# Kernel optimization log

Hardware: AMD Instinct MI355X
Metric: run time of the kernel (lower is better)

The kernel has to match this reference:

```python
import jax, jax.numpy as jnp
import numpy as np

B, T, D, H = 256, 512, 512, 512


def setup_inputs() -> dict:
    key = jax.random.key(0)
    k0, k1, k2, k3 = jax.random.split(key, 4)
    sD = 1.0 / np.sqrt(D).astype(np.float32)
    sH = 1.0 / np.sqrt(H).astype(np.float32)
    return {
        "x": jax.random.normal(k0, (B, T, D), jnp.float32),
        "Wx": jax.random.normal(k1, (D, 4 * H), jnp.float32) * sD,
        "Wh": jax.random.normal(k2, (H, 4 * H), jnp.float32) * sH,
        "b": jnp.zeros((4 * H,), jnp.float32),
        "Wfc": jax.random.normal(k3, (H, 1), jnp.float32) * sH,
        "bfc": jnp.zeros((1,), jnp.float32),
    }


def reference(x, Wx, Wh, b, Wfc, bfc):
    # x: [B, T, D]. Flax LSTMCell gates (i, f, g, o):
    #   i,f,o = sigmoid(.), g = tanh(.); c' = f*c + i*g; h' = o*tanh(c')
    Bv, Tv, _ = x.shape
    Hv = Wh.shape[0]
    # Precompute all input projections in one big GEMM (same math, batched).
    xg = jnp.einsum('btd,dg->btg', x, Wx) + b  # [B, T, 4H]

    def step(carry, xt):
        c, h = carry
        gates = xt + h @ Wh                     # [B, 4H]
        i, f, g, o = jnp.split(gates, 4, axis=-1)
        c_new = jax.nn.sigmoid(f) * c + jax.nn.sigmoid(i) * jnp.tanh(g)
        h_new = jax.nn.sigmoid(o) * jnp.tanh(c_new)
        return (c_new, h_new), None

    c0 = jnp.zeros((Bv, Hv), x.dtype)
    h0 = jnp.zeros((Bv, Hv), x.dtype)
    (c_fin, h_fin), _ = jax.lax.scan(step, (c0, h0), jnp.swapaxes(xg, 0, 1))
    # fc applied to last timestep output (== final hidden state)
    return h_fin @ Wfc + bfc  # [B, 1]
```

## Files before the change

### kernel.cpp

```cpp
#include <hip/hip_runtime.h>
#include <hip/hip_bf16.h>


typedef _Float16 half8 __attribute__((ext_vector_type(8)));
typedef _Float16 half4 __attribute__((ext_vector_type(4)));
typedef int int4v __attribute__((ext_vector_type(4)));
typedef float float4v __attribute__((ext_vector_type(4)));

__device__ __forceinline__ void gl_lds16(const void* g, void* l) {
  __builtin_amdgcn_global_load_lds(
      (const __attribute__((address_space(1))) unsigned int*)g,
      (__attribute__((address_space(3))) unsigned int*)l, 16, 0, 0);
}

__device__ __forceinline__ float sigm(float v) { return 1.f / (1.f + __expf(-v)); }
__device__ __forceinline__ float tanh_(float v) { return 1.f - 2.f / (__expf(2.f * v) + 1.f); }

__global__ __launch_bounds__(256) void k_prep(
    const float* __restrict__ x, const float* __restrict__ Wx,
    const float* __restrict__ Wh, const float* __restrict__ b,
    _Float16* __restrict__ xf, _Float16* __restrict__ wxt,
    _Float16* __restrict__ wht, float* __restrict__ bp)
{
  const long NX8 = 67108864L / 8;
  const long NW  = 2048L * 512;
  const long TOT = NX8 + 2 * NW + 2048;
  long stride = (long)gridDim.x * blockDim.x;
  for (long id = (long)blockIdx.x * blockDim.x + threadIdx.x; id < TOT; id += stride) {
    if (id < NX8) {
      const float4v* p = (const float4v*)x + id * 2;
      float4v a = p[0], c = p[1];
      half8 o;
      o[0]=(_Float16)a[0]; o[1]=(_Float16)a[1]; o[2]=(_Float16)a[2]; o[3]=(_Float16)a[3];
      o[4]=(_Float16)c[0]; o[5]=(_Float16)c[1]; o[6]=(_Float16)c[2]; o[7]=(_Float16)c[3];
      ((half8*)xf)[id] = o;
    } else if (id < NX8 + NW) {
      long e = id - NX8;
      int np = (int)(e >> 9), k = (int)(e & 511);
      int j = np >> 2, gt = np & 3;
      wxt[e] = (_Float16)Wx[(long)k * 2048 + gt * 512 + j];
    } else if (id < NX8 + 2 * NW) {
      long e = id - NX8 - NW;
      int np = (int)(e >> 9), k = (int)(e & 511);
      int j = np >> 2, gt = np & 3;
      wht[e] = (_Float16)Wh[(long)k * 2048 + gt * 512 + j];
    } else {
      int np = (int)(id - NX8 - 2 * NW);
      int j = np >> 2, gt = np & 3;
      bp[np] = b[gt * 512 + j];
    }
  }
}

__global__ __launch_bounds__(256, 2) void k_gemm_xg(
    const _Float16* __restrict__ xf, const _Float16* __restrict__ wxt,
    const float* __restrict__ bp, _Float16* __restrict__ xg)
{
  __shared__ _Float16 As[128 * 32];
  __shared__ _Float16 Bs[128 * 32];
  const int tid = threadIdx.x;
  const int w = tid >> 6, l = tid & 63;
  const int mt = blockIdx.x >> 4, nt = blockIdx.x & 15;
  const int qr = (w >> 1) * 64, qc = (w & 1) * 64;
  float4v acc[4][4];
  #pragma unroll
  for (int i = 0; i < 4; ++i)
    #pragma unroll
    for (int j = 0; j < 4; ++j) acc[i][j] = (float4v){0.f, 0.f, 0.f, 0.f};
  const int lr = l >> 2, lc = (l & 3) * 8;
  for (int kt = 0; kt < 16; ++kt) {
    __syncthreads();
    #pragma unroll
    for (int i = 0; i < 2; ++i) {
      int chunk = i * 4 + w;
      gl_lds16(xf + ((long)(mt * 128 + chunk * 16 + lr)) * 512 + kt * 32 + lc, As + chunk * 512);
      gl_lds16(wxt + ((long)(nt * 128 + chunk * 16 + lr)) * 512 + kt * 32 + lc, Bs + chunk * 512);
    }
    __syncthreads();
    half8 af[4], bf[4];
    #pragma unroll
    for (int mi = 0; mi < 4; ++mi)
      af[mi] = *(const half8*)(As + (qr + mi * 16 + (l & 15)) * 32 + (l >> 4) * 8);
    #pragma unroll
    for (int ni = 0; ni < 4; ++ni)
      bf[ni] = *(const half8*)(Bs + (qc + ni * 16 + (l & 15)) * 32 + (l >> 4) * 8);
    #pragma unroll
    for (int mi = 0; mi < 4; ++mi)
      #pragma unroll
      for (int ni = 0; ni < 4; ++ni)
        acc[mi][ni] = __builtin_amdgcn_mfma_f32_16x16x32_f16(af[mi], bf[ni], acc[mi][ni], 0, 0, 0);
  }
  #pragma unroll
  for (int ni = 0; ni < 4; ++ni) {
    int col = nt * 128 + qc + ni * 16 + (l & 15);
    float bias = bp[col];
    #pragma unroll
    for (int mi = 0; mi < 4; ++mi) {
      long R0 = (long)mt * 128 + qr + mi * 16 + (l >> 4) * 4;
      #pragma unroll
      for (int r = 0; r < 4; ++r)
        xg[(R0 + r) * 2048 + col] = (_Float16)(acc[mi][ni][r] + bias);
    }
  }
}

__global__ __launch_bounds__(256, 1) void k_scan(
    const _Float16* __restrict__ xg, const _Float16* __restrict__ wht,
    const float* __restrict__ wfc, const float* __restrict__ bfc,
    _Float16* __restrict__ hsl, unsigned int* __restrict__ flags,
    float* __restrict__ out)
{
  const int tid = threadIdx.x;
  const int w = tid >> 6, l = tid & 63;
  const int q = l >> 4;
  const int m = l & 15;
  const int bb = blockIdx.x;
  const int slot = bb >> 3;
  const int g = (bb & 7) * 2 + (slot >> 4);
  const int s = slot & 15;

  int4v bw0[16], bw1[16];
  {
    const _Float16* b0 = wht + ((long)(s * 128 + (2 * w + 0) * 16 + m)) * 512 + q * 8;
    const _Float16* b1 = wht + ((long)(s * 128 + (2 * w + 1) * 16 + m)) * 512 + q * 8;
    #pragma unroll
    for (int kk = 0; kk < 16; ++kk) {
      bw0[kk] = *(const int4v*)(b0 + kk * 32);
      bw1[kk] = *(const int4v*)(b1 + kk * 32);
    }
    #pragma unroll
    for (int kk = 0; kk < 16; ++kk)
      asm volatile("" : "+v"(bw0[kk]), "+v"(bw1[kk]));
  }

  float c0 = 0.f, c1 = 0.f;
  const int j0 = s * 32 + 8 * w + q;
  const int j1 = s * 32 + 8 * w + 4 + q;
  const float wf0 = wfc[j0], wf1 = wfc[j1];
  unsigned int* fl = flags + g * 256;
  const _Float16* xgr = xg + ((long)(g * 16 + m)) * 512 * 2048 + s * 128 + q * 4;
  const _Float16* hrg = hsl + (long)g * 8192 + q * 128 + m * 8;
  _Float16* hw = hsl + (long)(g * 16 + s) * 512 + w * 128 + m * 8;

  for (int t = 0; t < 512; ++t) {
    const int pr = t & 1;
    const half4 xv0 = *(const half4*)(xgr + (long)t * 2048 + (2 * w + 0) * 16);
    const half4 xv1 = *(const half4*)(xgr + (long)t * 2048 + (2 * w + 1) * 16);
    if (t) {
      if (w == 0 && l < 16) {
        unsigned int* p = fl + l * 16;
        while (__hip_atomic_load(p, __ATOMIC_RELAXED, __HIP_MEMORY_SCOPE_AGENT)
               < 4u * (unsigned)t) {}
      }
      asm volatile("" ::: "memory");
      __syncthreads();
    }
    const _Float16* hr = hrg + pr * 131072;
    int4v av[16];
    #pragma unroll
    for (int kk = 0; kk < 16; ++kk)
      asm volatile("global_load_dwordx4 %0, %1, off sc0 sc1"
                   : "=&v"(av[kk]) : "v"(hr + kk * 512) : "memory");
    asm volatile("s_waitcnt vmcnt(0)" ::: "memory");
    __builtin_amdgcn_sched_barrier(0);

    float4v a0 = (float4v){0.f,0.f,0.f,0.f}, a1 = a0, b0v = a0, b1v = a0;
    #pragma unroll
    for (int kk = 0; kk < 8; ++kk) {
      a0 = __builtin_amdgcn_mfma_f32_16x16x32_f16(__builtin_bit_cast(half8, bw0[kk]),
                                                  __builtin_bit_cast(half8, av[kk]), a0, 0, 0, 0);
      a1 = __builtin_amdgcn_mfma_f32_16x16x32_f16(__builtin_bit_cast(half8, bw1[kk]),
                                                  __builtin_bit_cast(half8, av[kk]), a1, 0, 0, 0);
    }
    #pragma unroll
    for (int kk = 8; kk < 16; ++kk) {
      b0v = __builtin_amdgcn_mfma_f32_16x16x32_f16(__builtin_bit_cast(half8, bw0[kk]),
                                                   __builtin_bit_cast(half8, av[kk]), b0v, 0, 0, 0);
      b1v = __builtin_amdgcn_mfma_f32_16x16x32_f16(__builtin_bit_cast(half8, bw1[kk]),
                                                   __builtin_bit_cast(half8, av[kk]), b1v, 0, 0, 0);
    }
    a0 += b0v; a1 += b1v;
    float i0 = sigm(a0[0] + (float)xv0[0]);
    float f0 = sigm(a0[1] + (float)xv0[1]);
    float g0 = tanh_(a0[2] + (float)xv0[2]);
    float o0 = sigm(a0[3] + (float)xv0[3]);
    c0 = f0 * c0 + i0 * g0;
    float h0v = o0 * tanh_(c0);
    float i1 = sigm(a1[0] + (float)xv1[0]);
    float f1 = sigm(a1[1] + (float)xv1[1]);
    float g1 = tanh_(a1[2] + (float)xv1[2]);
    float o1 = sigm(a1[3] + (float)xv1[3]);
    c1 = f1 * c1 + i1 * g1;
    float h1v = o1 * tanh_(c1);
    unsigned int hb0 = (unsigned int)__builtin_bit_cast(unsigned short, (_Float16)h0v);
    unsigned int hb1 = (unsigned int)__builtin_bit_cast(unsigned short, (_Float16)h1v);
    unsigned int pb0 = __shfl_xor(hb0, 16);
    unsigned int pb1 = __shfl_xor(hb1, 16);
    unsigned int pair0 = hb0 | (pb0 << 16);
    unsigned int pair1 = hb1 | (pb1 << 16);
    unsigned int x0 = __shfl_xor(pair0, 32);
    unsigned int x1 = __shfl_xor(pair1, 32);
    if (q == 0) {
      int4v pk = {(int)pair0, (int)x0, (int)pair1, (int)x1};
      _Float16* dst = hw + (pr ^ 1) * 131072;
      asm volatile("global_store_dwordx4 %0, %1, off sc0 sc1"
                   :: "v"(dst), "v"(pk) : "memory");
    }
    if (t == 511) {
      float part = h0v * wf0 + h1v * wf1;
      part += __shfl_xor(part, 16);
      part += __shfl_xor(part, 32);
      if (l < 16) {
        float v = part;
        if (s == 0 && w == 0) v += bfc[0];
        atomicAdd(out + g * 16 + l, v);
      }
    } else {
      asm volatile("s_waitcnt vmcnt(0)" ::: "memory");
      if (l == 0)
        (void)__hip_atomic_fetch_add(fl + s * 16, 1u, __ATOMIC_RELAXED,
                                     __HIP_MEMORY_SCOPE_AGENT);
    }
  }
}

extern "C" void kernel_launch(void* const* d_in, const int* in_sizes, int n_in,
                              void* d_out, int out_size, void* d_ws, size_t ws_size,
                              hipStream_t stream)
{
  const float* x   = (const float*)d_in[0];
  const float* Wx  = (const float*)d_in[1];
  const float* Wh  = (const float*)d_in[2];
  const float* b   = (const float*)d_in[3];
  const float* Wfc = (const float*)d_in[4];
  const float* bfc = (const float*)d_in[5];
  char* ws = (char*)d_ws;

  const size_t OFF_XG  = 0;
  const size_t OFF_XB  = 536870912UL;
  const size_t OFF_WXT = OFF_XB + 134217728UL;
  const size_t OFF_WHT = OFF_WXT + 2097152UL;
  const size_t OFF_BP  = OFF_WHT + 2097152UL;
  const size_t OFF_H   = OFF_BP + 8192UL;
  const size_t OFF_FL  = OFF_H + 524288UL;
  const size_t NEED    = OFF_FL + 16384UL;
  if (ws_size < NEED) return;

  _Float16* xgp = (_Float16*)(ws + OFF_XG);
  _Float16* xfp = (_Float16*)(ws + OFF_XB);
  _Float16* wxt = (_Float16*)(ws + OFF_WXT);
  _Float16* wht = (_Float16*)(ws + OFF_WHT);
  float*    bp  = (float*)(ws + OFF_BP);
  _Float16* hsl = (_Float16*)(ws + OFF_H);
  unsigned int* flg = (unsigned int*)(ws + OFF_FL);
  float* outp = (float*)d_out;

  hipMemsetAsync(ws + OFF_H, 0, 262144, stream);
  hipMemsetAsync(ws + OFF_FL, 0, 16384, stream);
  hipMemsetAsync(d_out, 0, sizeof(float) * 256, stream);

  k_prep<<<4096, 256, 0, stream>>>(x, Wx, Wh, b, xfp, wxt, wht, bp);
  k_gemm_xg<<<16384, 256, 0, stream>>>(xfp, wxt, bp, xgp);

  const _Float16* xgc = xgp;
  const _Float16* whtc = wht;
  void* args[] = { (void*)&xgc, (void*)&whtc, (void*)&Wfc, (void*)&bfc,
                   (void*)&hsl, (void*)&flg, (void*)&outp };
  hipLaunchCooperativeKernel((void*)k_scan, dim3(256), dim3(256), args, 0, stream);
}
```

Measured before the change: 1.868 ms.

## Aggregate per-wave step completion in LDS and prefetch next-step gate inputs

Each wave now increments a shared-memory counter after its hidden-state stores drain. Only the last of the four waves publishes the step number to the global flag with a plain atomic store, replacing four global fetch-adds per block per step. Waiters no longer spin on their own block's flag, relying on __syncthreads for intra-block ordering. The input-projection values for step t+1 are loaded one iteration ahead, taking that global load latency off the recurrent critical path.

```diff
diff --git a/kernel.cpp b/kernel.cpp
--- a/kernel.cpp
+++ b/kernel.cpp
@@ -110,7 +110,11 @@
     _Float16* __restrict__ hsl, unsigned int* __restrict__ flags,
     float* __restrict__ out)
 {
+  __shared__ unsigned int wctr;
   const int tid = threadIdx.x;
+  if (tid == 0) wctr = 0;
+  __syncthreads();
+
   const int w = tid >> 6, l = tid & 63;
   const int q = l >> 4;
   const int m = l & 15;
@@ -142,15 +146,19 @@
   const _Float16* hrg = hsl + (long)g * 8192 + q * 128 + m * 8;
   _Float16* hw = hsl + (long)(g * 16 + s) * 512 + w * 128 + m * 8;
 
+  half4 xc0 = *(const half4*)(xgr + (2 * w + 0) * 16);
+  half4 xc1 = *(const half4*)(xgr + (2 * w + 1) * 16);
+
   for (int t = 0; t < 512; ++t) {
     const int pr = t & 1;
-    const half4 xv0 = *(const half4*)(xgr + (long)t * 2048 + (2 * w + 0) * 16);
-    const half4 xv1 = *(const half4*)(xgr + (long)t * 2048 + (2 * w + 1) * 16);
+    const long tn = (t < 511) ? (long)(t + 1) : 511L;
+    const half4 xn0 = *(const half4*)(xgr + tn * 2048 + (2 * w + 0) * 16);
+    const half4 xn1 = *(const half4*)(xgr + tn * 2048 + (2 * w + 1) * 16);
     if (t) {
-      if (w == 0 && l < 16) {
+      if (w == 0 && l < 16 && l != s) {
         unsigned int* p = fl + l * 16;
         while (__hip_atomic_load(p, __ATOMIC_RELAXED, __HIP_MEMORY_SCOPE_AGENT)
-               < 4u * (unsigned)t) {}
+               < (unsigned)t) {}
       }
       asm volatile("" ::: "memory");
       __syncthreads();
@@ -180,16 +188,16 @@
                                                    __builtin_bit_cast(half8, av[kk]), b1v, 0, 0, 0);
     }
     a0 += b0v; a1 += b1v;
-    float i0 = sigm(a0[0] + (float)xv0[0]);
-    float f0 = sigm(a0[1] + (float)xv0[1]);
-    float g0 = tanh_(a0[2] + (float)xv0[2]);
-    float o0 = sigm(a0[3] + (float)xv0[3]);
+    float i0 = sigm(a0[0] + (float)xc0[0]);
+    float f0 = sigm(a0[1] + (float)xc0[1]);
+    float g0 = tanh_(a0[2] + (float)xc0[2]);
+    float o0 = sigm(a0[3] + (float)xc0[3]);
     c0 = f0 * c0 + i0 * g0;
     float h0v = o0 * tanh_(c0);
-    float i1 = sigm(a1[0] + (float)xv1[0]);
-    float f1 = sigm(a1[1] + (float)xv1[1]);
-    float g1 = tanh_(a1[2] + (float)xv1[2]);
-    float o1 = sigm(a1[3] + (float)xv1[3]);
+    float i1 = sigm(a1[0] + (float)xc1[0]);
+    float f1 = sigm(a1[1] + (float)xc1[1]);
+    float g1 = tanh_(a1[2] + (float)xc1[2]);
+    float o1 = sigm(a1[3] + (float)xc1[3]);
     c1 = f1 * c1 + i1 * g1;
     float h1v = o1 * tanh_(c1);
     unsigned int hb0 = (unsigned int)__builtin_bit_cast(unsigned short, (_Float16)h0v);
@@ -217,10 +225,14 @@
       }
     } else {
       asm volatile("s_waitcnt vmcnt(0)" ::: "memory");
-      if (l == 0)
-        (void)__hip_atomic_fetch_add(fl + s * 16, 1u, __ATOMIC_RELAXED,
-                                     __HIP_MEMORY_SCOPE_AGENT);
-    }
+      if (l == 0) {
+        unsigned int old = atomicAdd(&wctr, 1u);
+        if (old == 4u * (unsigned)t + 3u)
+          __hip_atomic_store(fl + s * 16, (unsigned)(t + 1),
+                             __ATOMIC_RELAXED, __HIP_MEMORY_SCOPE_AGENT);
+      }
+    }
+    xc0 = xn0; xc1 = xn1;
   }
 }
 
```

New measurement: 1.854 ms. About the same (-0.7%).
